# Kernel tuning notes

Measured on AMD Instinct MI355X. Metric: run time of the kernel, lower is better.

## Reference

```python
import math
import jax, jax.numpy as jnp
import numpy as np
from jax import lax

B, S, D = 2, 1024, 768
H, E, DH = 12, 8, 64          # n_head, num_experts, head dim
KA = 1                        # top-k experts per head (attention)
KF = 2                        # top-k experts per token (FFN)
DFF = 2048
EMA_DECAY = 0.99
CAP_FACTOR = 1.25
NEG_INF = -1e9


def setup_inputs() -> dict:
    key = jax.random.key(0)
    ks = jax.random.split(key, 16)
    sc = 0.02
    x = jax.random.normal(ks[0], (B, S, D), jnp.float32)
    causal = jnp.tril(jnp.ones((S, S), jnp.float32))
    mask = jnp.where(causal > 0, 0.0, NEG_INF).astype(jnp.float32)
    return {
        "x": x,
        "mask": mask,
        "W_q": jax.random.normal(ks[1], (D, D), jnp.float32) * sc,
        "W_k": jax.random.normal(ks[2], (D, D), jnp.float32) * sc,
        "W_v": jax.random.normal(ks[3], (H, E, DH, DH), jnp.float32) * sc,
        "W_o": jax.random.normal(ks[4], (H, E, DH, DH), jnp.float32) * sc,
        "W_router": jax.random.normal(ks[5], (D, H * E), jnp.float32) * sc,
        "g1": jnp.ones((D,), jnp.float32),
        "b1": jnp.zeros((D,), jnp.float32),
        "g2": jnp.ones((D,), jnp.float32),
        "b2": jnp.zeros((D,), jnp.float32),
        "gate_ff": jax.random.normal(ks[6], (D, E), jnp.float32) * sc,
        "W1": jax.random.normal(ks[7], (E, D, DFF), jnp.float32) * sc,
        "W2": jax.random.normal(ks[8], (E, DFF, D), jnp.float32) * sc,
    }


def layer_norm(x, g, b, eps=1e-5):
    m = jnp.mean(x, -1, keepdims=True)
    v = jnp.var(x, -1, keepdims=True)
    return (x - m) * lax.rsqrt(v + eps) * g + b


def head_switch_attention(x, mask, W_q, W_k, W_v, W_o, W_router):
    b, s, d = x.shape
    q = (x @ W_q).reshape(b, s, H, DH)
    k = (x @ W_k).reshape(b, s, H, DH)
    scores = jnp.einsum("bshd,bthd->bhst", q, k) / math.sqrt(DH) + mask
    p_attn = jax.nn.softmax(scores, axis=-1)          # (B,H,S,S)
    gate_logits = (x @ W_router).reshape(b, s, H, E)
    topk_scores, topk_idx = lax.top_k(gate_logits, KA)  # (B,S,H,KA)
    probs = jax.nn.softmax(topk_scores, axis=-1)
    x_h = x.reshape(b, s, H, DH)
    # value projections for all experts (small d_h x d_h GEMMs)
    v_all = jnp.einsum("bshd,hedf->bshef", x_h, W_v)
    y = jnp.zeros_like(x_h)
    hard_counts = jnp.zeros((H, E), jnp.float32)
    for slot in range(KA):
        oh = jax.nn.one_hot(topk_idx[..., slot], E, dtype=x.dtype)  # (B,S,H,E)
        v_sel = jnp.einsum("bshef,bshe->bshf", v_all, oh)
        # faithful to original einsum 'bhst,hbsd->hbtd' (sums over s)
        attn_out = jnp.einsum("bhst,bshf->bthf", p_attn, v_sel)
        o_all = jnp.einsum("bthf,hefg->btheg", attn_out, W_o)
        o_sel = jnp.einsum("btheg,bthe->bthg", o_all, oh)
        y = y + o_sel * probs[..., slot][..., None]
        hard_counts = hard_counts + lax.stop_gradient(oh).sum((0, 1))
    y = y.reshape(b, s, d)
    # EMA buffers start at zero -> ema = (1-decay)*hard/denom
    ema = hard_counts / (b * s * KA) * (1.0 - EMA_DECAY)
    p_lb = ema / (ema.sum() + 1e-9)
    aux = (p_lb * p_lb).sum() * E * H
    return y, aux


def moe_ffn(x, gate_ff, W1, W2):
    b, s, d = x.shape
    gate_logits = x @ gate_ff                      # (B,S,E), eval: no noise
    topk_scores, topk_idx = lax.top_k(gate_logits, KF)
    probs = jax.nn.softmax(topk_scores, axis=-1)   # (B,S,KF)
    capacity = math.ceil(CAP_FACTOR * (b * s) / E)
    flat_idx = topk_idx.reshape(-1)                # (B*S*KF,)
    oh_flat = jax.nn.one_hot(flat_idx, E, dtype=jnp.float32)
    tokens_so_far = jnp.cumsum(oh_flat, axis=0)
    keep = jnp.take_along_axis(tokens_so_far <= capacity, flat_idx[:, None], axis=1)[:, 0]
    probs = probs * keep.reshape(b, s, KF).astype(probs.dtype)
    probs = probs / (probs.sum(-1, keepdims=True) + 1e-9)
    oh = jax.nn.one_hot(topk_idx, E, dtype=probs.dtype)   # (B,S,KF,E)
    w = (probs[..., None] * oh).sum(2).reshape(b * s, E)  # combined weight per (token, expert)
    xf = x.reshape(b * s, d)
    yf = jnp.zeros_like(xf)
    for e in range(E):
        # scaling applied BEFORE ReLU, matching original x_sel = x * weight
        xe = xf * w[:, e:e + 1]
        yf = yf + jnp.maximum(xe @ W1[e], 0.0) @ W2[e]
    token_ctr = ((probs > 0)[..., None].astype(jnp.float32) * oh).sum((0, 1, 2))
    imp_ctr = (probs[..., None] * oh).sum((0, 1, 2))
    aux = ((token_ctr / token_ctr.sum()) * (imp_ctr / imp_ctr.sum())).sum() * E
    return yf.reshape(b, s, d), aux


def reference(x, mask, W_q, W_k, W_v, W_o, W_router, g1, b1, g2, b2, gate_ff, W1, W2):
    # pre-norm transformer block: x + Attn(LN(x)); x + MoEFFN(LN(x))
    a, aux1 = head_switch_attention(layer_norm(x, g1, b1), mask, W_q, W_k, W_v, W_o, W_router)
    x1 = x + a  # dropout is identity in eval
    f, aux2 = moe_ffn(layer_norm(x1, g2, b2), gate_ff, W1, W2)
    return x1 + f, aux1 + aux2
```

## Files before the change

kernel.cpp:

```cpp
#include <hip/hip_runtime.h>
#include <hip/hip_bf16.h>
#include <cstdint>

typedef __hip_bfloat16 bf16;
typedef __attribute__((ext_vector_type(8))) __bf16 bfrag;
typedef __attribute__((ext_vector_type(4))) float f32x4;

#define B_    2
#define S_    1024
#define D_    768
#define H_    12
#define E_    8
#define DH_   64
#define DFF_  2048
#define CAP_  320
#define CAPP_ 384
#define NTOK  (B_*S_)
#define NTH   (NTOK*H_)
#define QKLD  1536
#define NHE   (H_*E_)

__device__ __forceinline__ void stage16(const bf16* g, bf16* ldsLane){
#if __has_builtin(__builtin_amdgcn_global_load_lds)
  __builtin_amdgcn_global_load_lds((const __attribute__((address_space(1))) unsigned int*)g,
                                   (__attribute__((address_space(3))) unsigned int*)ldsLane, 16, 0, 0);
#else
  *(bfrag*)ldsLane = *(const bfrag*)g;
#endif
}

__device__ __forceinline__ void transp_tile_bf16(const float* __restrict__ src, bf16* __restrict__ dst,
                                                 int N, int K, int n0, int k0, int tid, float (*t)[64])
{
  int chunk = tid & 15, rgrp = tid >> 4;
#pragma unroll
  for (int rr=0; rr<8; rr++){
    int row = rr*16 + rgrp;
    float4 v = *(const float4*)(src + (long)(k0+row)*N + n0 + chunk*4);
    *(float4*)&t[row][((chunk ^ (row>>3)) & 15)*4] = v;
  }
  __syncthreads();
#pragma unroll
  for (int it=0; it<4; it++){
    int slot = it*256 + tid;
    int n = slot >> 4, kc = slot & 15;
    union { bfrag f; bf16 h[8]; } o;
#pragma unroll
    for (int i=0;i<8;i++){
      int row = kc*8 + i;
      o.h[i] = __float2bfloat16(t[row][n ^ (kc*4)]);
    }
    *(bfrag*)(dst + (long)(n0+n)*K + k0 + kc*8) = o.f;
  }
}

__global__ __launch_bounds__(256)
void transp_qkr(const float* __restrict__ Wq, const float* __restrict__ Wk,
                const float* __restrict__ Wr, bf16* __restrict__ WcatB, float* __restrict__ WrT)
{
  __shared__ float t[128][64];
  int bid = blockIdx.x, tid = threadIdx.x;
  if (bid < 144){
    const float* src; bf16* dst; int r;
    if (bid < 72){ src = Wq; dst = WcatB; r = bid; }
    else         { src = Wk; dst = WcatB + (long)768*768; r = bid - 72; }
    transp_tile_bf16(src, dst, 768, 768, (r%12)*64, (r/12)*128, tid, t);
  } else {
    int r = bid - 144;
    int n0 = (r % 3)*32, k0 = (r / 3)*64;
    int chunk = tid & 7, row2 = tid >> 3;
#pragma unroll
    for (int rr=0; rr<2; rr++){
      int row = rr*32 + row2;
      float4 v = *(const float4*)(Wr + (long)(k0+row)*96 + n0 + chunk*4);
      *(float4*)&t[row][chunk*4] = v;
    }
    __syncthreads();
    int chunkw = tid & 15, ng = tid >> 4;
#pragma unroll
    for (int rr=0; rr<2; rr++){
      int n = rr*16 + ng;
      float4 o;
      o.x = t[chunkw*4+0][n]; o.y = t[chunkw*4+1][n];
      o.z = t[chunkw*4+2][n]; o.w = t[chunkw*4+3][n];
      *(float4*)(WrT + (long)(n0+n)*768 + k0 + chunkw*4) = o;
    }
  }
}

__global__ __launch_bounds__(256)
void gemm_bn64(const bf16* __restrict__ A, const bf16* __restrict__ Bt,
               void* __restrict__ C, void* __restrict__ C2,
               int M, int N, int K, long sA, long sB, long sC, int relu, int outBf, int kSplit)
{
  int nwg = gridDim.x*gridDim.y*gridDim.z;
  int bid = blockIdx.x + gridDim.x*(blockIdx.y + gridDim.y*blockIdx.z);
  int nid = (bid & 7)*(nwg >> 3) + (bid >> 3);
  int bx = nid % gridDim.x;
  int t1 = nid / gridDim.x;
  int by = t1 % gridDim.y;
  int bz = t1 / gridDim.y;
  int e  = bz / kSplit, kc = bz - e*kSplit;
  A  += (long)e*sA;
  Bt += (long)e*sB;
  int kLen = K / kSplit, kBase = kc*kLen;
  int m0 = by*128, n0 = bx*64;
  __shared__ bf16 As[2][128*32];
  __shared__ bf16 Bs[2][64*32];
  int tid = threadIdx.x;
  int w = tid >> 6, lane = tid & 63;
  int quad = lane >> 4, l16 = lane & 15;
  int wm = w*32;
  f32x4 acc[2][4] = {};
  int srow = (lane >> 2);
  int gsw  = ((lane & 3) ^ (srow & 3))*8;
  const bf16* aBase = A + (long)m0*K;
  const bf16* bBase = Bt + (long)n0*K;
  int xr = (l16 & 3);
  int nIt = kLen >> 5;
  {
    int k0 = kBase;
#pragma unroll
    for (int j=0;j<2;j++){
      int c = w*2 + j, row = c*16 + srow;
      stage16(aBase + (long)row*K + k0 + gsw, As[0] + c*512 + lane*8);
    }
    int rowb = w*16 + srow;
    stage16(bBase + (long)rowb*K + k0 + gsw, Bs[0] + w*512 + lane*8);
  }
  int cur = 0;
  for (int it=0; it<nIt; ++it){
    __syncthreads();
    if (it+1 < nIt){
      int k0 = kBase + (it+1)*32;
      int nb = cur^1;
#pragma unroll
      for (int j=0;j<2;j++){
        int c = w*2 + j, row = c*16 + srow;
        stage16(aBase + (long)row*K + k0 + gsw, As[nb] + c*512 + lane*8);
      }
      int rowb = w*16 + srow;
      stage16(bBase + (long)rowb*K + k0 + gsw, Bs[nb] + w*512 + lane*8);
    }
    const bf16* Ac = As[cur];
    const bf16* Bc = Bs[cur];
    bfrag af[2], bfv[4];
#pragma unroll
    for (int t=0;t<2;t++) af[t]  = *(const bfrag*)(Ac + (wm + t*16 + l16)*32 + ((quad ^ xr)*8));
#pragma unroll
    for (int t=0;t<4;t++) bfv[t] = *(const bfrag*)(Bc + (t*16 + l16)*32 + ((quad ^ xr)*8));
#pragma unroll
    for (int ti=0;ti<2;ti++)
#pragma unroll
      for (int tj=0;tj<4;tj++)
        acc[ti][tj] = __builtin_amdgcn_mfma_f32_16x16x32_bf16(af[ti], bfv[tj], acc[ti][tj], 0, 0, 0);
    cur ^= 1;
  }
  long zoff = (long)e*sC;
  void* Cp = kc ? C2 : C;
  if (outBf){
    bf16* Cb = (bf16*)Cp + zoff;
#pragma unroll
    for (int ti=0;ti<2;ti++)
#pragma unroll
      for (int tj=0;tj<4;tj++)
#pragma unroll
        for (int r=0;r<4;r++){
          int row = m0 + wm + ti*16 + quad*4 + r;
          int col = n0 + tj*16 + l16;
          float v = acc[ti][tj][r];
          if (relu) v = fmaxf(v, 0.f);
          Cb[(long)row*N + col] = __float2bfloat16(v);
        }
  } else {
    float* Cf = (float*)Cp + zoff;
#pragma unroll
    for (int ti=0;ti<2;ti++)
#pragma unroll
      for (int tj=0;tj<4;tj++)
#pragma unroll
        for (int r=0;r<4;r++){
          int row = m0 + wm + ti*16 + quad*4 + r;
          int col = n0 + tj*16 + l16;
          float v = acc[ti][tj][r];
          if (relu) v = fmaxf(v, 0.f);
          Cf[(long)row*N + col] = v;
        }
  }
}

__global__ __launch_bounds__(256)
void gemm_ffn1(const float* __restrict__ ln2, const bf16* __restrict__ Bt, bf16* __restrict__ C,
               const int* __restrict__ lTok, const float* __restrict__ lW, const int* __restrict__ gCnt)
{
  int nwg = gridDim.x*gridDim.y*gridDim.z;
  int bid = blockIdx.x + gridDim.x*(blockIdx.y + gridDim.y*blockIdx.z);
  int nid = (bid & 7)*(nwg >> 3) + (bid >> 3);
  int bx = nid % gridDim.x;
  int t1 = nid / gridDim.x;
  int by = t1 % gridDim.y;
  int e  = t1 / gridDim.y;
  int m0 = by*128;
  const bf16* bBase = Bt + (long)e*2048*768 + (long)(bx*64)*768;
  __shared__ bf16 As[2][128*32];
  __shared__ bf16 Bs[2][64*32];
  int tid = threadIdx.x;
  int w = tid >> 6, lane = tid & 63;
  int quad = lane >> 4, l16 = lane & 15;
  int wm = w*32;
  f32x4 acc[2][4] = {};
  int srow = (lane >> 2);
  int gsw  = ((lane & 3) ^ (srow & 3))*8;
  int xr = (l16 & 3);
  int cnt = gCnt[e];
  int tokA[2]; float wA[2];
#pragma unroll
  for (int j=0;j<2;j++){
    int row = m0 + (w*2+j)*16 + srow;
    bool live = row < cnt;
    tokA[j] = live ? lTok[e*CAP_ + row] : 0;
    wA[j]   = live ? lW[e*CAP_ + row]   : 0.f;
  }
  const int nIt = 24;
  {
#pragma unroll
    for (int j=0;j<2;j++){
      const float* src = ln2 + (long)tokA[j]*D_ + gsw;
      float4 a0 = *(const float4*)(src);
      float4 a1 = *(const float4*)(src+4);
      union { bfrag f; bf16 h[8]; } o;
      o.h[0]=__float2bfloat16(a0.x*wA[j]); o.h[1]=__float2bfloat16(a0.y*wA[j]);
      o.h[2]=__float2bfloat16(a0.z*wA[j]); o.h[3]=__float2bfloat16(a0.w*wA[j]);
      o.h[4]=__float2bfloat16(a1.x*wA[j]); o.h[5]=__float2bfloat16(a1.y*wA[j]);
      o.h[6]=__float2bfloat16(a1.z*wA[j]); o.h[7]=__float2bfloat16(a1.w*wA[j]);
      *(bfrag*)(As[0] + (w*2+j)*512 + lane*8) = o.f;
    }
    int rowb = w*16 + srow;
    stage16(bBase + (long)rowb*768 + gsw, Bs[0] + w*512 + lane*8);
  }
  int cur = 0;
  for (int it=0; it<nIt; ++it){
    __syncthreads();
    float4 a0[2], a1[2];
    if (it+1 < nIt){
      int k0 = (it+1)*32;
#pragma unroll
      for (int j=0;j<2;j++){
        const float* src = ln2 + (long)tokA[j]*D_ + k0 + gsw;
        a0[j] = *(const float4*)(src);
        a1[j] = *(const float4*)(src+4);
      }
      int rowb = w*16 + srow;
      stage16(bBase + (long)rowb*768 + k0 + gsw, Bs[cur^1] + w*512 + lane*8);
    }
    const bf16* Ac = As[cur];
    const bf16* Bc = Bs[cur];
    bfrag af[2], bfv[4];
#pragma unroll
    for (int t=0;t<2;t++) af[t]  = *(const bfrag*)(Ac + (wm + t*16 + l16)*32 + ((quad ^ xr)*8));
#pragma unroll
    for (int t=0;t<4;t++) bfv[t] = *(const bfrag*)(Bc + (t*16 + l16)*32 + ((quad ^ xr)*8));
#pragma unroll
    for (int ti=0;ti<2;ti++)
#pragma unroll
      for (int tj=0;tj<4;tj++)
        acc[ti][tj] = __builtin_amdgcn_mfma_f32_16x16x32_bf16(af[ti], bfv[tj], acc[ti][tj], 0, 0, 0);
    if (it+1 < nIt){
      int nb = cur^1;
#pragma unroll
      for (int j=0;j<2;j++){
        union { bfrag f; bf16 h[8]; } o;
        o.h[0]=__float2bfloat16(a0[j].x*wA[j]); o.h[1]=__float2bfloat16(a0[j].y*wA[j]);
        o.h[2]=__float2bfloat16(a0[j].z*wA[j]); o.h[3]=__float2bfloat16(a0[j].w*wA[j]);
        o.h[4]=__float2bfloat16(a1[j].x*wA[j]); o.h[5]=__float2bfloat16(a1[j].y*wA[j]);
        o.h[6]=__float2bfloat16(a1[j].z*wA[j]); o.h[7]=__float2bfloat16(a1[j].w*wA[j]);
        *(bfrag*)(As[nb] + (w*2+j)*512 + lane*8) = o.f;
      }
    }
    cur ^= 1;
  }
  bf16* Cb = C + (long)e*CAPP_*DFF_;
#pragma unroll
  for (int ti=0;ti<2;ti++)
#pragma unroll
    for (int tj=0;tj<4;tj++)
#pragma unroll
      for (int r=0;r<4;r++){
        int row = m0 + wm + ti*16 + quad*4 + r;
        int col = bx*64 + tj*16 + l16;
        Cb[(long)row*DFF_ + col] = __float2bfloat16(fmaxf(acc[ti][tj][r], 0.f));
      }
}

__global__ __launch_bounds__(256)
void ln_kernel(const float* __restrict__ src, const float* __restrict__ g, const float* __restrict__ bb,
               float* __restrict__ dstF, bf16* __restrict__ dstB,
               const float* __restrict__ gateW, float* __restrict__ glog2)
{
  int row = blockIdx.x, tid = threadIdx.x;
  __shared__ float red[256];
  __shared__ float gsum[4][E_];
  float v[3];
#pragma unroll
  for (int j=0;j<3;j++) v[j] = src[(long)row*D_ + tid + j*256];
  float s = v[0]+v[1]+v[2];
  red[tid]=s; __syncthreads();
  for (int o=128;o>0;o>>=1){ if(tid<o) red[tid]+=red[tid+o]; __syncthreads(); }
  float mean = red[0]*(1.0f/D_);
  __syncthreads();
  float sq = 0.f;
#pragma unroll
  for (int j=0;j<3;j++){ float d=v[j]-mean; sq += d*d; }
  red[tid]=sq; __syncthreads();
  for (int o=128;o>0;o>>=1){ if(tid<o) red[tid]+=red[tid+o]; __syncthreads(); }
  float rstd = rsqrtf(red[0]*(1.0f/D_) + 1e-5f);
  float ov[3];
#pragma unroll
  for (int j=0;j<3;j++){
    int d = tid + j*256;
    float o = (v[j]-mean)*rstd*g[d] + bb[d];
    ov[j] = o;
    dstF[(long)row*D_+d] = o;
    if (dstB) dstB[(long)row*D_+d] = __float2bfloat16(o);
  }
  if (gateW){
    float gp[E_] = {};
#pragma unroll
    for (int j=0;j<3;j++){
      int d = tid + j*256;
      const float* gw = gateW + (long)d*E_;
#pragma unroll
      for (int e=0;e<E_;e++) gp[e] += ov[j]*gw[e];
    }
#pragma unroll
    for (int off=1; off<64; off<<=1)
#pragma unroll
      for (int e=0;e<E_;e++) gp[e] += __shfl_xor(gp[e], off);
    if ((tid & 63) == 0)
#pragma unroll
      for (int e=0;e<E_;e++) gsum[tid>>6][e] = gp[e];
    __syncthreads();
    if (tid < E_)
      glog2[(long)row*E_ + tid] = gsum[0][tid]+gsum[1][tid]+gsum[2][tid]+gsum[3][tid];
  }
}

#define RTOK 4
__global__ __launch_bounds__(768)
void router_argmax(const float* __restrict__ ln1, const float* __restrict__ WrT,
                   int* __restrict__ eidx, int* __restrict__ gHist,
                   int* __restrict__ hCnt, int* __restrict__ hList)
{
  int tok0 = blockIdx.x*RTOK;
  int tid = threadIdx.x;
  int col = tid >> 3, seg = tid & 7;
  __shared__ float xrow[RTOK][D_];
  __shared__ float logits[RTOK][96];
  for (int i=tid; i<RTOK*D_; i+=768){
    int t = i / D_, dpos = i - t*D_;
    xrow[t][dpos] = ln1[(long)(tok0+t)*D_ + dpos];
  }
  __syncthreads();
  const float* wrow = WrT + (long)col*D_;
  float acc[RTOK] = {};
#pragma unroll
  for (int j=0;j<24;j++){
    int dbase = j*32 + seg*4;
    float4 w = *(const float4*)(wrow + dbase);
#pragma unroll
    for (int t=0;t<RTOK;t++){
      float4 xv = *(const float4*)(&xrow[t][dbase]);
      acc[t] += xv.x*w.x + xv.y*w.y + xv.z*w.z + xv.w*w.w;
    }
  }
#pragma unroll
  for (int off=1; off<8; off<<=1)
#pragma unroll
    for (int t=0;t<RTOK;t++) acc[t] += __shfl_xor(acc[t], off);
  if (seg == 0)
#pragma unroll
    for (int t=0;t<RTOK;t++) logits[t][col] = acc[t];
  __syncthreads();
  if (tid < RTOK*H_){
    int t = tid / H_, h = tid % H_;
    const float* p = &logits[t][h*8];
    float best = p[0]; int bi = 0;
#pragma unroll
    for (int e=1;e<8;e++){ float v=p[e]; if (v > best){ best=v; bi=e; } }
    int tok = tok0 + t;
    eidx[tok*H_ + h] = bi;
    atomicAdd(&gHist[h*E_ + bi], 1);
    int he = h*E_ + bi;
    int pos = atomicAdd(&hCnt[he], 1);
    hList[he*NTOK + pos] = tok;
  }
}

__global__ __launch_bounds__(256)
void vsel_b(const float* __restrict__ ln1, const float* __restrict__ Wv,
            const int* __restrict__ hCnt, const int* __restrict__ hList,
            bf16* __restrict__ vT)
{
  int he = blockIdx.x;
  int h = he >> 3;
  __shared__ float Ws[DH_*DH_];
  __shared__ float xsh[4][DH_];
  int tid = threadIdx.x;
  const float* W = Wv + (long)he*DH_*DH_;
  for (int i=tid; i<DH_*DH_; i+=256) Ws[i] = W[i];
  int cnt = hCnt[he];
  __syncthreads();
  int w = tid >> 6, lane = tid & 63;
  const int* lst = hList + (long)he*NTOK;
  for (int i = blockIdx.y*4 + w; i < cnt; i += 32){
    int tok = lst[i];
    int b = tok >> 10, s = tok & 1023;
    xsh[w][lane] = ln1[(long)tok*D_ + h*DH_ + lane];
    float acc = 0.f;
#pragma unroll 8
    for (int d=0; d<DH_; d++) acc += xsh[w][d]*Ws[d*DH_ + lane];
    vT[((long)(b*H_+h)*DH_ + lane)*S_ + s] = __float2bfloat16(acc);
  }
}

__global__ __launch_bounds__(256)
void attn_stats_mfma(const bf16* __restrict__ qkB, float* __restrict__ gM, float* __restrict__ gL,
                     const float* __restrict__ W1, bf16* __restrict__ WT1)
{
  __shared__ __align__(16) char smem[32768];
  int tid = threadIdx.x;
  if (blockIdx.z >= 2){
    int flat = (blockIdx.z - 2)*96 + blockIdx.y*8 + blockIdx.x;
    int e = flat/192, r = flat - e*192;
    transp_tile_bf16(W1 + (long)e*768*2048, WT1 + (long)e*2048*768, 2048, 768,
                     (r % 32)*64, (r / 32)*128, tid, (float(*)[64])smem);
    return;
  }
  bf16* ldsQ = (bf16*)smem;
  int h = blockIdx.y, b = blockIdx.z;
  int w = tid >> 6, lane = tid & 63;
  int quad = lane >> 4, l16 = lane & 15;
  int x7 = l16 & 7;
  const bf16* kbase = qkB + ((long)(b*S_))*QKLD + 768 + h*DH_;
  for (int half=0; half<2; half++){
    int s0 = (half ? (S_/64 - 1 - blockIdx.x) : blockIdx.x)*64;
    __syncthreads();
    const bf16* qbase = qkB + ((long)(b*S_ + s0))*QKLD + h*DH_;
#pragma unroll
    for (int j=0;j<2;j++){
      int c = j*256 + tid;
      int row = c >> 3;
      int gs = ((c & 7) ^ (row & 7))*8;
      stage16(qbase + (long)row*QKLD + gs, ldsQ + c*8);
      stage16(kbase + (long)row*QKLD + gs, (bf16*)(smem + 8192) + c*8);
    }
    float m_ln[4] = {-1e30f,-1e30f,-1e30f,-1e30f};
    float l_ln[4] = {0.f,0.f,0.f,0.f};
    int ttEnd = s0 >> 6;
    int cur = 0;
    for (int tt=0; tt<=ttEnd; tt++){
      __syncthreads();
      if (tt < ttEnd){
        bf16* Kn = (bf16*)(smem + 8192 + ((cur^1) << 13));
#pragma unroll
        for (int j=0;j<2;j++){
          int c = j*256 + tid;
          int row = c >> 3;
          int gs = ((c & 7) ^ (row & 7))*8;
          stage16(kbase + (long)((tt+1)*64 + row)*QKLD + gs, Kn + c*8);
        }
      }
      const bf16* Kc = (const bf16*)(smem + 8192 + (cur << 13));
      bfrag af0 = *(const bfrag*)(ldsQ + (w*16 + l16)*64 + ((quad     ^ x7)*8));
      bfrag af1 = *(const bfrag*)(ldsQ + (w*16 + l16)*64 + (((quad+4) ^ x7)*8));
      f32x4 cfr[4];
#pragma unroll
      for (int j=0;j<4;j++){
        bfrag b0 = *(const bfrag*)(Kc + (j*16 + l16)*64 + ((quad     ^ x7)*8));
        bfrag b1 = *(const bfrag*)(Kc + (j*16 + l16)*64 + (((quad+4) ^ x7)*8));
        f32x4 z = {};
        z = __builtin_amdgcn_mfma_f32_16x16x32_bf16(af0, b0, z, 0,0,0);
        z = __builtin_amdgcn_mfma_f32_16x16x32_bf16(af1, b1, z, 0,0,0);
        cfr[j] = z;
      }
#pragma unroll
      for (int r=0;r<4;r++){
        int s_g = s0 + w*16 + quad*4 + r;
        float v0 = (tt*64      + l16 <= s_g) ? cfr[0][r]*0.125f : -1e30f;
        float v1 = (tt*64 + 16 + l16 <= s_g) ? cfr[1][r]*0.125f : -1e30f;
        float v2 = (tt*64 + 32 + l16 <= s_g) ? cfr[2][r]*0.125f : -1e30f;
        float v3 = (tt*64 + 48 + l16 <= s_g) ? cfr[3][r]*0.125f : -1e30f;
        float mt = fmaxf(fmaxf(v0,v1), fmaxf(v2,v3));
        float mn = fmaxf(m_ln[r], mt);
        l_ln[r] = l_ln[r]*__expf(m_ln[r]-mn)
                + ((__expf(v0-mn)+__expf(v1-mn)) + (__expf(v2-mn)+__expf(v3-mn)));
        m_ln[r] = mn;
      }
      cur ^= 1;
    }
#pragma unroll
    for (int r=0;r<4;r++){
      float mf = m_ln[r];
#pragma unroll
      for (int mm=1; mm<16; mm<<=1) mf = fmaxf(mf, __shfl_xor(mf, mm));
      float lf = l_ln[r]*__expf(m_ln[r]-mf);
#pragma unroll
      for (int mm=1; mm<16; mm<<=1) lf += __shfl_xor(lf, mm);
      if (l16 == 0){
        long basei = ((long)(b*H_ + h))*S_ + s0 + w*16 + quad*4 + r;
        gM[basei] = mf; gL[basei] = lf;
      }
    }
  }
}

__global__ __launch_bounds__(256)
void attn_pv(const bf16* __restrict__ qkB, const bf16* __restrict__ vT,
             const float* __restrict__ gM, const float* __restrict__ gL, float* __restrict__ aoH,
             const float* __restrict__ W2, bf16* __restrict__ WT2)
{
  __shared__ __align__(16) char smem[51200];
  int tid = threadIdx.x;
  if (blockIdx.z >= 2){
    int flat = (blockIdx.z - 2)*96 + blockIdx.y*8 + blockIdx.x;
    int e = flat/192, r = flat - e*192;
    transp_tile_bf16(W2 + (long)e*2048*768, WT2 + (long)e*768*2048, 768, 2048,
                     (r % 12)*64, (r / 12)*128, tid, (float(*)[64])smem);
    return;
  }
  bf16* ldsK = (bf16*)smem;
  bf16* ldsS = (bf16*)(smem + 40960);
  float* smxB = (float*)(smem + 50176);
  float* sliB = (float*)(smem + 50688);
  int h = blockIdx.y, b = blockIdx.z;
  int bh = b*H_ + h;
  int w = tid >> 6, lane = tid & 63;
  int quad = lane >> 4, l16 = lane & 15;
  int x7 = l16 & 7;
  const bf16* qbase = qkB + ((long)(b*S_))*QKLD + h*DH_;
  const bf16* vbase = vT + ((long)bh*DH_)*S_;
  for (int half=0; half<2; half++){
    int t0 = (half ? (S_/64 - 1 - blockIdx.x) : blockIdx.x)*64;
    __syncthreads();
    const bf16* kbase = qkB + ((long)(b*S_ + t0))*QKLD + 768 + h*DH_;
    int sb0 = t0 >> 6;
#pragma unroll
    for (int j=0;j<2;j++){
      int c = j*256 + tid;
      int row = c >> 3;
      int gs = ((c & 7) ^ (row & 7))*8;
      stage16(kbase + (long)row*QKLD + gs, ldsK + c*8);
      stage16(qbase + (long)(sb0*64 + row)*QKLD + gs, (bf16*)(smem + 8192) + c*8);
      stage16(vbase + (long)row*S_ + sb0*64 + gs, (bf16*)(smem + 24576) + c*8);
    }
    if (tid < 64){
      smxB[tid] = gM[(long)bh*S_ + sb0*64 + tid];
      sliB[tid] = 1.0f / gL[(long)bh*S_ + sb0*64 + tid];
    }
    f32x4 accO[4] = {};
    int cur = 0;
    for (int sb = sb0; sb < S_/64; sb++){
      __syncthreads();
      if (sb+1 < S_/64){
        int nb = cur^1;
        bf16* Qn = (bf16*)(smem + 8192 + (nb << 13));
        bf16* Vn = (bf16*)(smem + 24576 + (nb << 13));
#pragma unroll
        for (int j=0;j<2;j++){
          int c = j*256 + tid;
          int row = c >> 3;
          int gs = ((c & 7) ^ (row & 7))*8;
          stage16(qbase + (long)((sb+1)*64 + row)*QKLD + gs, Qn + c*8);
          stage16(vbase + (long)row*S_ + (sb+1)*64 + gs, Vn + c*8);
        }
        if (tid < 64){
          smxB[nb*64 + tid] = gM[(long)bh*S_ + (sb+1)*64 + tid];
          sliB[nb*64 + tid] = 1.0f / gL[(long)bh*S_ + (sb+1)*64 + tid];
        }
      }
      const bf16* Qc = (const bf16*)(smem + 8192 + (cur << 13));
      const bf16* Vc = (const bf16*)(smem + 24576 + (cur << 13));
      bfrag af0 = *(const bfrag*)(ldsK + (w*16 + l16)*64 + ((quad     ^ x7)*8));
      bfrag af1 = *(const bfrag*)(ldsK + (w*16 + l16)*64 + (((quad+4) ^ x7)*8));
      f32x4 cs[4];
#pragma unroll
      for (int j=0;j<4;j++){
        bfrag b0 = *(const bfrag*)(Qc + (j*16 + l16)*64 + ((quad     ^ x7)*8));
        bfrag b1 = *(const bfrag*)(Qc + (j*16 + l16)*64 + (((quad+4) ^ x7)*8));
        f32x4 z = {};
        z = __builtin_amdgcn_mfma_f32_16x16x32_bf16(af0, b0, z, 0,0,0);
        z = __builtin_amdgcn_mfma_f32_16x16x32_bf16(af1, b1, z, 0,0,0);
        cs[j] = z;
      }
#pragma unroll
      for (int j=0;j<4;j++)
#pragma unroll
        for (int r=0;r<4;r++){
          int t_loc = w*16 + quad*4 + r;
          int s_loc = j*16 + l16;
          float wgt = ((t0 + t_loc) <= (sb*64 + s_loc))
                    ? __expf(cs[j][r]*0.125f - smxB[cur*64 + s_loc])*sliB[cur*64 + s_loc] : 0.f;
          ldsS[t_loc*72 + s_loc] = __float2bfloat16(wgt);
        }
      bfrag pa0 = *(const bfrag*)(ldsS + (w*16 + l16)*72 + quad*8);
      bfrag pa1 = *(const bfrag*)(ldsS + (w*16 + l16)*72 + 32 + quad*8);
#pragma unroll
      for (int j=0;j<4;j++){
        bfrag b0 = *(const bfrag*)(Vc + (j*16 + l16)*64 + ((quad     ^ x7)*8));
        bfrag b1 = *(const bfrag*)(Vc + (j*16 + l16)*64 + (((quad+4) ^ x7)*8));
        accO[j] = __builtin_amdgcn_mfma_f32_16x16x32_bf16(pa0, b0, accO[j], 0,0,0);
        accO[j] = __builtin_amdgcn_mfma_f32_16x16x32_bf16(pa1, b1, accO[j], 0,0,0);
      }
      cur ^= 1;
    }
#pragma unroll
    for (int j=0;j<4;j++)
#pragma unroll
      for (int r=0;r<4;r++){
        int t_loc = w*16 + quad*4 + r;
        int f = j*16 + l16;
        aoH[((long)bh*S_ + t0 + t_loc)*DH_ + f] = accO[j][r];
      }
  }
}

__global__ __launch_bounds__(256)
void oproj_b(const float* __restrict__ aoH, const float* __restrict__ Wo,
             const int* __restrict__ hCnt, const int* __restrict__ hList,
             const float* __restrict__ x, float* __restrict__ x1)
{
  int he = blockIdx.x;
  int h = he >> 3;
  __shared__ float Ws[DH_*DH_];
  __shared__ float xsh[4][DH_];
  int tid = threadIdx.x;
  const float* W = Wo + (long)he*DH_*DH_;
  for (int i=tid; i<DH_*DH_; i+=256) Ws[i] = W[i];
  int cnt = hCnt[he];
  __syncthreads();
  int w = tid >> 6, lane = tid & 63;
  const int* lst = hList + (long)he*NTOK;
  for (int i = blockIdx.y*4 + w; i < cnt; i += 32){
    int tok = lst[i];
    int b = tok >> 10, s = tok & 1023;
    xsh[w][lane] = aoH[((long)(b*H_+h)*S_ + s)*DH_ + lane];
    float acc = 0.f;
#pragma unroll 8
    for (int f=0; f<DH_; f++) acc += xsh[w][f]*Ws[f*DH_ + lane];
    long idx = (long)tok*D_ + h*DH_ + lane;
    x1[idx] = x[idx] + acc;
  }
}

__global__ __launch_bounds__(1024)
void route_kernel(const float* __restrict__ glog2, const int* __restrict__ gHist,
                  int* __restrict__ gI0, int* __restrict__ gI1,
                  int* __restrict__ gPos0, int* __restrict__ gPos1,
                  int* __restrict__ listTok, float* __restrict__ listW,
                  int* __restrict__ gCnt, float* __restrict__ auxOut)
{
  __shared__ unsigned char sI0[NTOK], sI1[NTOK];
  __shared__ float sP0[NTOK], sP1[NTOK];
  __shared__ short sPos0[NTOK], sPos1[NTOK];
  __shared__ int   waveTot[16][E_];
  __shared__ float waveImp[16][E_];
  __shared__ float sImp[E_];
  __shared__ int   sHist[NHE];
  __shared__ int   sCnt[E_];
  int tid = threadIdx.x;
  int lane = tid & 63, wv = tid >> 6;
  if (tid < NHE) sHist[tid] = gHist[tid];
  for (int i=tid; i<NTOK; i+=1024){
    const float* p = glog2 + (long)i*E_;
    float b0 = p[0]; int e0 = 0;
#pragma unroll
    for (int e=1;e<E_;e++){ float vv=p[e]; if (vv > b0){ b0=vv; e0=e; } }
    float b1v = -1e30f; int e1 = 0;
#pragma unroll
    for (int e=0;e<E_;e++){ if (e==e0) continue; float vv=p[e]; if (vv > b1v){ b1v=vv; e1=e; } }
    float ex = __expf(b1v - b0);
    float inv = 1.f/(1.f + ex);
    sI0[i] = (unsigned char)e0; sI1[i] = (unsigned char)e1;
    sP0[i] = inv; sP1[i] = ex*inv;
    gI0[i] = e0; gI1[i] = e1;
  }
  __syncthreads();
  int myCnt[E_] = {};
  unsigned char ie[4];
  int base = tid*4;
#pragma unroll
  for (int j=0;j<4;j++){
    int i = base + j;
    int tok = i >> 1;
    int e = (i & 1) ? (int)sI1[tok] : (int)sI0[tok];
    ie[j] = (unsigned char)e;
#pragma unroll
    for (int ee=0;ee<E_;ee++) myCnt[ee] += (e == ee);
  }
  int inc[E_];
#pragma unroll
  for (int e=0;e<E_;e++) inc[e] = myCnt[e];
#pragma unroll
  for (int off=1; off<64; off<<=1){
#pragma unroll
    for (int e=0;e<E_;e++){
      int v = __shfl_up(inc[e], off);
      if (lane >= off) inc[e] += v;
    }
  }
  if (lane == 63)
#pragma unroll
    for (int e=0;e<E_;e++) waveTot[wv][e] = inc[e];
  __syncthreads();
  int pref[E_];
#pragma unroll
  for (int e=0;e<E_;e++) pref[e] = inc[e] - myCnt[e];
  for (int w2=0; w2<16; w2++){
    if (w2 < wv){
#pragma unroll
      for (int e=0;e<E_;e++) pref[e] += waveTot[w2][e];
    }
  }
#pragma unroll
  for (int j=0;j<4;j++){
    int i = base + j;
    int tok = i >> 1;
    int pos = 0;
#pragma unroll
    for (int ee=0;ee<E_;ee++) if (ie[j] == ee) pos = pref[ee]++;
    short p = (pos < CAP_) ? (short)pos : (short)-1;
    if (i & 1) sPos1[tok] = p; else sPos0[tok] = p;
  }
  if (tid < E_){
    int cnt = 0;
    for (int w2=0; w2<16; w2++) cnt += waveTot[w2][tid];
    sCnt[tid] = cnt < CAP_ ? cnt : CAP_;
    gCnt[tid] = sCnt[tid];
  }
  __syncthreads();
  float impLoc[E_] = {};
  for (int i=tid; i<NTOK; i+=1024){
    int e0 = sI0[i], e1 = sI1[i];
    int p0i = sPos0[i], p1i = sPos1[i];
    float k0 = p0i >= 0 ? 1.f : 0.f, k1 = p1i >= 0 ? 1.f : 0.f;
    float p0 = sP0[i], p1 = sP1[i];
    float denom = p0*k0 + p1*k1 + 1e-9f;
    float w0 = p0*k0/denom, w1 = p1*k1/denom;
    if (p0i >= 0){
      listTok[e0*CAP_+p0i] = i; listW[e0*CAP_+p0i] = w0;
#pragma unroll
      for (int ee=0;ee<E_;ee++) impLoc[ee] += (e0 == ee) ? w0 : 0.f;
    }
    if (p1i >= 0){
      listTok[e1*CAP_+p1i] = i; listW[e1*CAP_+p1i] = w1;
#pragma unroll
      for (int ee=0;ee<E_;ee++) impLoc[ee] += (e1 == ee) ? w1 : 0.f;
    }
    gPos0[i] = p0i; gPos1[i] = p1i;
  }
#pragma unroll
  for (int off=1; off<64; off<<=1)
#pragma unroll
    for (int e=0;e<E_;e++) impLoc[e] += __shfl_xor(impLoc[e], off);
  if (lane == 0)
#pragma unroll
    for (int e=0;e<E_;e++) waveImp[wv][e] = impLoc[e];
  __syncthreads();
  if (tid < E_){
    float s = 0.f;
    for (int w2=0; w2<16; w2++) s += waveImp[w2][tid];
    sImp[tid] = s;
  }
  __syncthreads();
  if (tid == 0){
    float tot = 0.f;
    for (int i=0;i<NHE;i++) tot += (float)sHist[i]*(1.0f/NTOK)*0.01f;
    float a1 = 0.f;
    for (int i=0;i<NHE;i++){
      float p = ((float)sHist[i]*(1.0f/NTOK)*0.01f)/(tot + 1e-9f);
      a1 += p*p;
    }
    a1 *= (float)(H_*E_);
    float tcs = 0.f, ims = 0.f;
    for (int e=0;e<E_;e++){ tcs += (float)sCnt[e]; ims += sImp[e]; }
    float a2 = 0.f;
    for (int e=0;e<E_;e++) a2 += ((float)sCnt[e]/tcs)*(sImp[e]/ims);
    a2 *= (float)E_;
    auxOut[0] = a1 + a2;
  }
}

__global__ __launch_bounds__(256)
void combine_kernel(const float* __restrict__ x1,
                    const float* __restrict__ Ya, const float* __restrict__ Yb,
                    const int* __restrict__ gI0, const int* __restrict__ gI1,
                    const int* __restrict__ gPos0, const int* __restrict__ gPos1,
                    float* __restrict__ out)
{
  int i = blockIdx.x;
  int tid = threadIdx.x;
  int p0 = gPos0[i], p1 = gPos1[i];
  int e0 = gI0[i],  e1 = gI1[i];
  long off0 = (long)(e0*CAPP_ + (p0 >= 0 ? p0 : 0))*D_;
  long off1 = (long)(e1*CAPP_ + (p1 >= 0 ? p1 : 0))*D_;
  const float* y0a = Ya + off0; const float* y0b = Yb + off0;
  const float* y1a = Ya + off1; const float* y1b = Yb + off1;
  for (int d=tid; d<D_; d+=256){
    float v = x1[(long)i*D_+d];
    if (p0 >= 0) v += y0a[d] + y0b[d];
    if (p1 >= 0) v += y1a[d] + y1b[d];
    out[(long)i*D_+d] = v;
  }
}

extern "C" void kernel_launch(void* const* d_in, const int* in_sizes, int n_in,
                              void* d_out, int out_size, void* d_ws, size_t ws_size,
                              hipStream_t stream)
{
  const float* x    = (const float*)d_in[0];
  const float* W_q  = (const float*)d_in[2];
  const float* W_k  = (const float*)d_in[3];
  const float* W_v  = (const float*)d_in[4];
  const float* W_o  = (const float*)d_in[5];
  const float* W_r  = (const float*)d_in[6];
  const float* g1   = (const float*)d_in[7];
  const float* b1   = (const float*)d_in[8];
  const float* g2   = (const float*)d_in[9];
  const float* b2   = (const float*)d_in[10];
  const float* gate = (const float*)d_in[11];
  const float* W1   = (const float*)d_in[12];
  const float* W2   = (const float*)d_in[13];
  float* out = (float*)d_out;

  float* wsf = (float*)d_ws;
  const long oX1   = 0;
  const long oLnF  = 1572864;
  const long oLnB  = 3145728;
  const long oWcat = 3932160;
  const long oWrT  = 4521984;
  const long oHist = 4595712;
  const long oHCnt = 4595808;
  const long oGM   = 4718592;
  const long oGL   = 4743168;
  const long oEidx = 4767744;
  const long oGlg2 = 4792320;
  const long oI0   = 4808704;
  const long oI1   = 4810752;
  const long oP0   = 4812800;
  const long oP1   = 4814848;
  const long oLT   = 4816896;
  const long oLW   = 4819456;
  const long oCnt  = 4822016;
  const long SB    = 4822528;
  const long oWT1  = SB + 12976128;
  const long oWT2  = oWT1 + 6291456;
  const long TOTAL = oWT2 + 6291456;
  if (ws_size < (size_t)TOTAL*4) return;

  float* x1    = wsf + oX1;
  float* lnbF  = wsf + oLnF;
  bf16*  lnbB  = (bf16*)(wsf + oLnB);
  bf16*  WcatB = (bf16*)(wsf + oWcat);
  float* WrT   = wsf + oWrT;
  int*   gHist = (int*)(wsf + oHist);
  int*   hCnt  = (int*)(wsf + oHCnt);
  float* gM    = wsf + oGM;
  float* gL    = wsf + oGL;
  int*   eidx  = (int*)(wsf + oEidx);
  float* glog2 = wsf + oGlg2;
  int*   gI0   = (int*)(wsf + oI0);
  int*   gI1   = (int*)(wsf + oI1);
  int*   gPos0 = (int*)(wsf + oP0);
  int*   gPos1 = (int*)(wsf + oP1);
  int*   lTok  = (int*)(wsf + oLT);
  float* lW    = wsf + oLW;
  int*   gCnt  = (int*)(wsf + oCnt);
  bf16*  qkB   = (bf16*)(wsf + SB);
  bf16*  vT    = (bf16*)(wsf + SB + 1572864);
  float* aoH   = wsf + SB + 2359296;
  int*   hList = (int*)(wsf + SB + 3932160);
  bf16*  Hid   = (bf16*)(wsf + SB + 7471104);
  float* Yexp  = wsf + SB + 10616832;
  float* YexpB = wsf + oLnF;
  bf16*  WT1   = (bf16*)(wsf + oWT1);
  bf16*  WT2   = (bf16*)(wsf + oWT2);

  (void)hipMemsetAsync(gHist, 0, 2*NHE*sizeof(int), stream);
  transp_qkr<<<180,256,0,stream>>>(W_q, W_k, W_r, WcatB, WrT);

  ln_kernel<<<NTOK,256,0,stream>>>(x, g1, b1, lnbF, lnbB, nullptr, nullptr);
  gemm_bn64<<<dim3(24,16,1),256,0,stream>>>(lnbB, WcatB, qkB, nullptr, 2048, QKLD, 768, 0,0,0, 0, 1, 1);
  router_argmax<<<NTOK/RTOK,768,0,stream>>>(lnbF, WrT, eidx, gHist, hCnt, hList);
  vsel_b<<<dim3(NHE,8,1),256,0,stream>>>(lnbF, W_v, hCnt, hList, vT);
  attn_stats_mfma<<<dim3(S_/128,H_,2+16),256,0,stream>>>(qkB, gM, gL, W1, WT1);
  attn_pv<<<dim3(S_/128,H_,2+16),256,0,stream>>>(qkB, vT, gM, gL, aoH, W2, WT2);
  oproj_b<<<dim3(NHE,8,1),256,0,stream>>>(aoH, W_o, hCnt, hList, x, x1);

  ln_kernel<<<NTOK,256,0,stream>>>(x1, g2, b2, lnbF, nullptr, gate, glog2);
  route_kernel<<<1,1024,0,stream>>>(glog2, gHist, gI0,gI1,gPos0,gPos1, lTok,lW,gCnt, out + (size_t)NTOK*D_);
  gemm_ffn1<<<dim3(32,3,8),256,0,stream>>>(lnbF, WT1, Hid, lTok, lW, gCnt);
  gemm_bn64<<<dim3(12,3,16),256,0,stream>>>(Hid, WT2, Yexp, YexpB, CAPP_, 768, 2048,
                                            (long)CAPP_*2048, (long)768*2048, (long)CAPP_*768, 0, 0, 2);
  combine_kernel<<<NTOK,256,0,stream>>>(x1, Yexp, YexpB, gI0,gI1,gPos0,gPos1, out);
}
```

Measured before the change: 378.5 us.

## Fuse router argmax into QK GEMM launch and vsel into attention stats

```diff
diff --git a/kernel.cpp b/kernel.cpp
--- a/kernel.cpp
+++ b/kernel.cpp
@@ -86,6 +86,129 @@
       *(float4*)(WrT + (long)(n0+n)*768 + k0 + chunkw*4) = o;
     }
   }
+}
+
+#define RTOK 4
+__global__ __launch_bounds__(256)
+void gemm_qk(const bf16* __restrict__ A, const bf16* __restrict__ Bt, bf16* __restrict__ C,
+             const float* __restrict__ ln1, const float* __restrict__ WrT,
+             int* __restrict__ eidx, int* __restrict__ gHist,
+             int* __restrict__ hCnt, int* __restrict__ hList)
+{
+  __shared__ __align__(16) char smem[24576];
+  int tid = threadIdx.x;
+  if (blockIdx.z >= 1){
+    int flat = (blockIdx.z - 1)*384 + blockIdx.y*24 + blockIdx.x;
+    if (flat >= NTOK/RTOK) return;
+    int tok0 = flat*RTOK;
+    float* xrow = (float*)smem;
+    float* logits = (float*)(smem + 12288);
+#pragma unroll
+    for (int k=0;k<3;k++){
+      int idx = tid + k*256;
+      int t = idx / 192, dpos = (idx - t*192)*4;
+      *(float4*)&xrow[t*768 + dpos] = *(const float4*)(ln1 + (long)(tok0+t)*D_ + dpos);
+    }
+    __syncthreads();
+    int col = tid >> 1, seg = tid & 1;
+    if (col < 96){
+      const float* wrow = WrT + (long)col*D_;
+      float acc[RTOK] = {};
+#pragma unroll
+      for (int j=0;j<96;j++){
+        int dbase = j*8 + seg*4;
+        float4 w = *(const float4*)(wrow + dbase);
+#pragma unroll
+        for (int t=0;t<RTOK;t++){
+          float4 xv = *(const float4*)(&xrow[t*768 + dbase]);
+          acc[t] += xv.x*w.x + xv.y*w.y + xv.z*w.z + xv.w*w.w;
+        }
+      }
+#pragma unroll
+      for (int t=0;t<RTOK;t++) acc[t] += __shfl_xor(acc[t], 1);
+      if (seg == 0)
+#pragma unroll
+        for (int t=0;t<RTOK;t++) logits[t*96 + col] = acc[t];
+    }
+    __syncthreads();
+    if (tid < RTOK*H_){
+      int t = tid / H_, h = tid % H_;
+      const float* p = &logits[t*96 + h*8];
+      float best = p[0]; int bi = 0;
+#pragma unroll
+      for (int e=1;e<8;e++){ float v=p[e]; if (v > best){ best=v; bi=e; } }
+      int tok = tok0 + t;
+      eidx[tok*H_ + h] = bi;
+      atomicAdd(&gHist[h*E_ + bi], 1);
+      int he = h*E_ + bi;
+      int pos = atomicAdd(&hCnt[he], 1);
+      hList[he*NTOK + pos] = tok;
+    }
+    return;
+  }
+  int bid = blockIdx.x + 24*blockIdx.y;
+  int nid = (bid & 7)*48 + (bid >> 3);
+  int bx = nid % 24, by = nid / 24;
+  int m0 = by*128, n0 = bx*64;
+  int w = tid >> 6, lane = tid & 63;
+  int quad = lane >> 4, l16 = lane & 15;
+  int wm = w*32;
+  f32x4 acc[2][4] = {};
+  int srow = (lane >> 2);
+  int gsw  = ((lane & 3) ^ (srow & 3))*8;
+  const bf16* aBase = A + (long)m0*768;
+  const bf16* bBase = Bt + (long)n0*768;
+  int xr = (l16 & 3);
+  const int nIt = 24;
+  {
+#pragma unroll
+    for (int j=0;j<2;j++){
+      int c = w*2 + j, row = c*16 + srow;
+      stage16(aBase + (long)row*768 + gsw, (bf16*)smem + c*512 + lane*8);
+    }
+    int rowb = w*16 + srow;
+    stage16(bBase + (long)rowb*768 + gsw, (bf16*)(smem + 16384) + w*512 + lane*8);
+  }
+  int cur = 0;
+  for (int it=0; it<nIt; ++it){
+    __syncthreads();
+    if (it+1 < nIt){
+      int k0 = (it+1)*32;
+      int nb = cur^1;
+      bf16* An = (bf16*)(smem + (nb<<13));
+      bf16* Bn = (bf16*)(smem + 16384 + (nb<<12));
+#pragma unroll
+      for (int j=0;j<2;j++){
+        int c = w*2 + j, row = c*16 + srow;
+        stage16(aBase + (long)row*768 + k0 + gsw, An + c*512 + lane*8);
+      }
+      int rowb = w*16 + srow;
+      stage16(bBase + (long)rowb*768 + k0 + gsw, Bn + w*512 + lane*8);
+    }
+    const bf16* Ac = (const bf16*)(smem + (cur<<13));
+    const bf16* Bc = (const bf16*)(smem + 16384 + (cur<<12));
+    bfrag af[2], bfv[4];
+#pragma unroll
+    for (int t=0;t<2;t++) af[t]  = *(const bfrag*)(Ac + (wm + t*16 + l16)*32 + ((quad ^ xr)*8));
+#pragma unroll
+    for (int t=0;t<4;t++) bfv[t] = *(const bfrag*)(Bc + (t*16 + l16)*32 + ((quad ^ xr)*8));
+#pragma unroll
+    for (int ti=0;ti<2;ti++)
+#pragma unroll
+      for (int tj=0;tj<4;tj++)
+        acc[ti][tj] = __builtin_amdgcn_mfma_f32_16x16x32_bf16(af[ti], bfv[tj], acc[ti][tj], 0, 0, 0);
+    cur ^= 1;
+  }
+#pragma unroll
+  for (int ti=0;ti<2;ti++)
+#pragma unroll
+    for (int tj=0;tj<4;tj++)
+#pragma unroll
+      for (int r=0;r<4;r++){
+        int row = m0 + wm + ti*16 + quad*4 + r;
+        int col = n0 + tj*16 + l16;
+        C[(long)row*QKLD + col] = __float2bfloat16(acc[ti][tj][r]);
+      }
 }
 
 __global__ __launch_bounds__(256)
@@ -345,90 +468,38 @@
   }
 }
 
-#define RTOK 4
-__global__ __launch_bounds__(768)
-void router_argmax(const float* __restrict__ ln1, const float* __restrict__ WrT,
-                   int* __restrict__ eidx, int* __restrict__ gHist,
-                   int* __restrict__ hCnt, int* __restrict__ hList)
-{
-  int tok0 = blockIdx.x*RTOK;
-  int tid = threadIdx.x;
-  int col = tid >> 3, seg = tid & 7;
-  __shared__ float xrow[RTOK][D_];
-  __shared__ float logits[RTOK][96];
-  for (int i=tid; i<RTOK*D_; i+=768){
-    int t = i / D_, dpos = i - t*D_;
-    xrow[t][dpos] = ln1[(long)(tok0+t)*D_ + dpos];
-  }
-  __syncthreads();
-  const float* wrow = WrT + (long)col*D_;
-  float acc[RTOK] = {};
-#pragma unroll
-  for (int j=0;j<24;j++){
-    int dbase = j*32 + seg*4;
-    float4 w = *(const float4*)(wrow + dbase);
-#pragma unroll
-    for (int t=0;t<RTOK;t++){
-      float4 xv = *(const float4*)(&xrow[t][dbase]);
-      acc[t] += xv.x*w.x + xv.y*w.y + xv.z*w.z + xv.w*w.w;
-    }
-  }
-#pragma unroll
-  for (int off=1; off<8; off<<=1)
-#pragma unroll
-    for (int t=0;t<RTOK;t++) acc[t] += __shfl_xor(acc[t], off);
-  if (seg == 0)
-#pragma unroll
-    for (int t=0;t<RTOK;t++) logits[t][col] = acc[t];
-  __syncthreads();
-  if (tid < RTOK*H_){
-    int t = tid / H_, h = tid % H_;
-    const float* p = &logits[t][h*8];
-    float best = p[0]; int bi = 0;
-#pragma unroll
-    for (int e=1;e<8;e++){ float v=p[e]; if (v > best){ best=v; bi=e; } }
-    int tok = tok0 + t;
-    eidx[tok*H_ + h] = bi;
-    atomicAdd(&gHist[h*E_ + bi], 1);
-    int he = h*E_ + bi;
-    int pos = atomicAdd(&hCnt[he], 1);
-    hList[he*NTOK + pos] = tok;
-  }
-}
-
-__global__ __launch_bounds__(256)
-void vsel_b(const float* __restrict__ ln1, const float* __restrict__ Wv,
-            const int* __restrict__ hCnt, const int* __restrict__ hList,
-            bf16* __restrict__ vT)
-{
-  int he = blockIdx.x;
-  int h = he >> 3;
-  __shared__ float Ws[DH_*DH_];
-  __shared__ float xsh[4][DH_];
-  int tid = threadIdx.x;
-  const float* W = Wv + (long)he*DH_*DH_;
-  for (int i=tid; i<DH_*DH_; i+=256) Ws[i] = W[i];
-  int cnt = hCnt[he];
-  __syncthreads();
-  int w = tid >> 6, lane = tid & 63;
-  const int* lst = hList + (long)he*NTOK;
-  for (int i = blockIdx.y*4 + w; i < cnt; i += 32){
-    int tok = lst[i];
-    int b = tok >> 10, s = tok & 1023;
-    xsh[w][lane] = ln1[(long)tok*D_ + h*DH_ + lane];
-    float acc = 0.f;
-#pragma unroll 8
-    for (int d=0; d<DH_; d++) acc += xsh[w][d]*Ws[d*DH_ + lane];
-    vT[((long)(b*H_+h)*DH_ + lane)*S_ + s] = __float2bfloat16(acc);
-  }
-}
-
 __global__ __launch_bounds__(256)
 void attn_stats_mfma(const bf16* __restrict__ qkB, float* __restrict__ gM, float* __restrict__ gL,
-                     const float* __restrict__ W1, bf16* __restrict__ WT1)
+                     const float* __restrict__ W1, bf16* __restrict__ WT1,
+                     const float* __restrict__ ln1, const float* __restrict__ Wv,
+                     const int* __restrict__ hCnt, const int* __restrict__ hList,
+                     bf16* __restrict__ vT)
 {
   __shared__ __align__(16) char smem[32768];
   int tid = threadIdx.x;
+  if (blockIdx.z >= 18){
+    int vs = blockIdx.z - 18;
+    int he = blockIdx.y*8 + blockIdx.x;
+    int h = he >> 3;
+    float* Ws  = (float*)smem;
+    float* xsh = (float*)(smem + 16384);
+    const float* W = Wv + (long)he*DH_*DH_;
+    for (int i=tid; i<DH_*DH_; i+=256) Ws[i] = W[i];
+    int cnt = hCnt[he];
+    __syncthreads();
+    int w = tid >> 6, lane = tid & 63;
+    const int* lst = hList + (long)he*NTOK;
+    for (int i = vs*4 + w; i < cnt; i += 32){
+      int tok = lst[i];
+      int b = tok >> 10, s = tok & 1023;
+      xsh[w*64 + lane] = ln1[(long)tok*D_ + h*DH_ + lane];
+      float acc = 0.f;
+#pragma unroll 8
+      for (int d=0; d<DH_; d++) acc += xsh[w*64 + d]*Ws[d*DH_ + lane];
+      vT[((long)(b*H_+h)*DH_ + lane)*S_ + s] = __float2bfloat16(acc);
+    }
+    return;
+  }
   if (blockIdx.z >= 2){
     int flat = (blockIdx.z - 2)*96 + blockIdx.y*8 + blockIdx.x;
     int e = flat/192, r = flat - e*192;
@@ -889,11 +960,9 @@
   transp_qkr<<<180,256,0,stream>>>(W_q, W_k, W_r, WcatB, WrT);
 
   ln_kernel<<<NTOK,256,0,stream>>>(x, g1, b1, lnbF, lnbB, nullptr, nullptr);
-  gemm_bn64<<<dim3(24,16,1),256,0,stream>>>(lnbB, WcatB, qkB, nullptr, 2048, QKLD, 768, 0,0,0, 0, 1, 1);
-  router_argmax<<<NTOK/RTOK,768,0,stream>>>(lnbF, WrT, eidx, gHist, hCnt, hList);
-  vsel_b<<<dim3(NHE,8,1),256,0,stream>>>(lnbF, W_v, hCnt, hList, vT);
-  attn_stats_mfma<<<dim3(S_/128,H_,2+16),256,0,stream>>>(qkB, gM, gL, W1, WT1);
-  attn_pv<<<dim3(S_/128,H_,2+16),256,0,stream>>>(qkB, vT, gM, gL, aoH, W2, WT2);
+  gemm_qk<<<dim3(24,16,3),256,0,stream>>>(lnbB, WcatB, qkB, lnbF, WrT, eidx, gHist, hCnt, hList);
+  attn_stats_mfma<<<dim3(S_/128,H_,26),256,0,stream>>>(qkB, gM, gL, W1, WT1, lnbF, W_v, hCnt, hList, vT);
+  attn_pv<<<dim3(S_/128,H_,18),256,0,stream>>>(qkB, vT, gM, gL, aoH, W2, WT2);
   oproj_b<<<dim3(NHE,8,1),256,0,stream>>>(aoH, W_o, hCnt, hList, x, x1);
 
   ln_kernel<<<NTOK,256,0,stream>>>(x1, g2, b2, lnbF, nullptr, gate, glog2);
```

New measurement: 362.9 us. -4.1%, faster.
